# Kernel tuning notes

Measured on AMD Instinct MI355X. Metric: run time of the kernel, lower is better.

The kernel has to match this reference:

```python
import jax, jax.numpy as jnp
import numpy as np

N = 50000
IN_DIM = 512
HIDDEN = 64
OUT_DIM = 47
E1 = 800000
E2 = 1200000


def setup_inputs() -> dict:
    key = jax.random.key(0)
    ks = jax.random.split(key, 10)
    x = jax.random.normal(ks[0], (N, IN_DIM), dtype=jnp.float32)
    src1 = jax.random.randint(ks[1], (E1,), 0, N, dtype=jnp.int32)
    dst1 = jax.random.randint(ks[2], (E1,), 0, N, dtype=jnp.int32)
    w1 = jax.random.uniform(ks[3], (E1,), dtype=jnp.float32)
    src2 = jax.random.randint(ks[4], (E2,), 0, N, dtype=jnp.int32)
    dst2 = jax.random.randint(ks[5], (E2,), 0, N, dtype=jnp.int32)
    w2 = jax.random.uniform(ks[6], (E2,), dtype=jnp.float32)
    embed_w = jax.random.normal(ks[7], (IN_DIM, HIDDEN), dtype=jnp.float32) / np.sqrt(IN_DIM)
    embed_b = jnp.zeros((HIDDEN,), dtype=jnp.float32)
    total_dim = (2 ** 3 - 1) * HIDDEN  # k=2 -> 7*hidden
    cls_w = jax.random.normal(ks[8], (total_dim, OUT_DIM), dtype=jnp.float32) / np.sqrt(total_dim)
    cls_b = jnp.zeros((OUT_DIM,), dtype=jnp.float32)
    return {"x": x, "src1": src1, "dst1": dst1, "w1": w1,
            "src2": src2, "dst2": dst2, "w2": w2,
            "embed_w": embed_w, "embed_b": embed_b,
            "cls_w": cls_w, "cls_b": cls_b}


def _spmm(src, dst, w, h, n):
    # out[i] = sum_{e: dst[e]==i} w[e] * h[src[e]]  == sparse_adj @ h
    return jax.ops.segment_sum(w[:, None] * h[src], dst, num_segments=n)


def reference(x, src1, dst1, w1, src2, dst2, w2, embed_w, embed_b, cls_w, cls_b):
    k = 2
    # dropout is identity in eval mode
    h = jax.nn.relu(x @ embed_w + embed_b)  # [N, hidden]
    reps = [h]
    for _ in range(k):
        h1 = _spmm(src1, dst1, w1, h, N)  # strict 1-hop
        h2 = _spmm(src2, dst2, w2, h, N)  # strict 2-hop
        h = jax.nn.relu(jnp.concatenate([h1, h2], axis=1))
        reps.append(h)
    h_final = jnp.concatenate(reps, axis=1)  # [N, 7*hidden]
    return h_final @ cls_w + cls_b
```

## Files before the change

kernel.cpp:

```cpp
#include <hip/hip_runtime.h>

#define N_NODES 50000
#define IN_DIM 512
#define HIDDEN 64
#define OUT_DIM 47
#define HSTRIDE 448

#define NBINS 391
#define CAP1 3072
#define CAP2 4096
#define CHUNK 4096

typedef unsigned short u16;
typedef short v8s __attribute__((ext_vector_type(8)));
typedef float v4f __attribute__((ext_vector_type(4)));

union F4 { float4 v; float f[4]; };
union U4 { uint4 v; unsigned u[4]; };

static __device__ __forceinline__ u16 f2bf(float f) {
  unsigned u = __float_as_uint(f);
  u += 0x7fffu + ((u >> 16) & 1u);
  return (u16)(u >> 16);
}
static __device__ __forceinline__ float bf2f(u16 h) {
  return __uint_as_float(((unsigned)h) << 16);
}

__global__ __launch_bounds__(256) void prep_scatter(
    const float* __restrict__ embed_w, u16* __restrict__ weTh,
    u16* __restrict__ weTl, const float* __restrict__ cls_w,
    u16* __restrict__ wcTh, u16* __restrict__ wcTl,
    const int* __restrict__ src1, const int* __restrict__ dst1,
    const float* __restrict__ w1, int E1, int c1,
    const int* __restrict__ src2, const int* __restrict__ dst2,
    const float* __restrict__ w2, int E2,
    int* __restrict__ binCursor, int2* __restrict__ stg1,
    int2* __restrict__ stg2) {
  int b = blockIdx.x;
  if (b < 16) {
    int tid = b * 256 + threadIdx.x;
    int col = tid >> 6;
    int k8 = (tid & 63) * 8;
#pragma unroll
    for (int j = 0; j < 8; j++) {
      float v = embed_w[(size_t)(k8 + j) * HIDDEN + col];
      u16 h = f2bf(v);
      weTh[(size_t)col * IN_DIM + k8 + j] = h;
      weTl[(size_t)col * IN_DIM + k8 + j] = f2bf(v - bf2f(h));
    }
    return;
  }
  if (b < 27) {
    int tid = (b - 16) * 256 + threadIdx.x;
    if (tid < 48 * 56) {
      int col = tid / 56;
      int k8 = (tid % 56) * 8;
#pragma unroll
      for (int j = 0; j < 8; j++) {
        float v = (col < OUT_DIM) ? cls_w[(size_t)(k8 + j) * OUT_DIM + col] : 0.f;
        u16 h = f2bf(v);
        wcTh[(size_t)col * HSTRIDE + k8 + j] = h;
        wcTl[(size_t)col * HSTRIDE + k8 + j] = f2bf(v - bf2f(h));
      }
    }
    return;
  }

  int q = b - 27;
  const int *src, *dst;
  const float* w;
  int E, cap;
  int2* stg;
  int* bc;
  if (q < c1) {
    src = src1; dst = dst1; w = w1; E = E1; stg = stg1; bc = binCursor; cap = CAP1;
  } else {
    q -= c1;
    src = src2; dst = dst2; w = w2; E = E2; stg = stg2; bc = binCursor + NBINS; cap = CAP2;
  }
  int e0 = q * CHUNK;
  int n = E - e0;
  if (n > CHUNK) n = CHUNK;

  __shared__ int hist[NBINS], segrel[NBINS], cur[NBINS];
  for (int i = threadIdx.x; i < NBINS; i += 256) { hist[i] = 0; cur[i] = 0; }
  __syncthreads();
  for (int t = threadIdx.x; t < n; t += 256)
    atomicAdd(&hist[dst[e0 + t] >> 7], 1);
  __syncthreads();
  for (int i = threadIdx.x; i < NBINS; i += 256) {
    int h = hist[i];
    segrel[i] = h ? atomicAdd(&bc[i], h) : 0;
  }
  __syncthreads();
  for (int t = threadIdx.x; t < n; t += 256) {
    int d = dst[e0 + t];
    int bin = d >> 7;
    int rel = segrel[bin] + atomicAdd(&cur[bin], 1);
    if (rel < cap)
      stg[(size_t)bin * cap + rel] =
          make_int2(src[e0 + t] | ((d & 127) << 16), __float_as_int(w[e0 + t]));
  }
}

__global__ __launch_bounds__(512) void binscan(const int* __restrict__ cnt,
                                               int* __restrict__ scanout) {
  const int* in = cnt + blockIdx.x * NBINS;
  int* out = scanout + blockIdx.x * NBINS;
  int tid = threadIdx.x, lane = tid & 63, wid = tid >> 6;
  __shared__ int wsum[8];
  int v0 = (tid < NBINS) ? in[tid] : 0;
  int v = v0;
#pragma unroll
  for (int off = 1; off < 64; off <<= 1) {
    int t = __shfl_up(v, off, 64);
    if (lane >= off) v += t;
  }
  if (lane == 63) wsum[wid] = v;
  __syncthreads();
  if (tid < 8) {
    int s = wsum[tid], sc = s;
#pragma unroll
    for (int off = 1; off < 8; off <<= 1) {
      int t = __shfl_up(sc, off, 8);
      if (tid >= off) sc += t;
    }
    wsum[tid] = sc - s;
  }
  __syncthreads();
  if (tid < NBINS) out[tid] = v - v0 + wsum[wid];
}

__global__ __launch_bounds__(256) void embed_place(
    const float* __restrict__ x, const u16* __restrict__ wTh,
    const u16* __restrict__ wTl, const float* __restrict__ bias,
    u16* __restrict__ hcat, const int* __restrict__ binCursor,
    const int* __restrict__ binScan, const int2* __restrict__ stg1,
    int2* __restrict__ ew1, int* __restrict__ ep1,
    const int2* __restrict__ stg2, int2* __restrict__ ew2,
    int* __restrict__ ep2) {
  int b = blockIdx.x;
  if (b < 782) {
    int wave = threadIdx.x >> 6, lane = threadIdx.x & 63;
    int row0 = b * 64 + wave * 16;
    int m = lane & 15, kq = lane >> 4;
    int rowA = row0 + m;
    if (rowA >= N_NODES) rowA = N_NODES - 1;
    const float* xr = x + (size_t)rowA * IN_DIM;

    v4f acc[4];
#pragma unroll
    for (int nf = 0; nf < 4; nf++) acc[nf] = (v4f){0.f, 0.f, 0.f, 0.f};

#pragma unroll 4
    for (int k0 = 0; k0 < IN_DIM; k0 += 32) {
      int kk = k0 + kq * 8;
      F4 p, qv;
      p.v = *(const float4*)(xr + kk);
      qv.v = *(const float4*)(xr + kk + 4);
      v8s a;
#pragma unroll
      for (int j = 0; j < 4; j++) {
        a[j] = (short)f2bf(p.f[j]);
        a[4 + j] = (short)f2bf(qv.f[j]);
      }
#pragma unroll
      for (int nf = 0; nf < 4; nf++) {
        int col = nf * 16 + m;
        v8s bh = *(const v8s*)(wTh + (size_t)col * IN_DIM + kk);
        v8s bl = *(const v8s*)(wTl + (size_t)col * IN_DIM + kk);
        acc[nf] = __builtin_amdgcn_mfma_f32_16x16x32_bf16(a, bh, acc[nf], 0, 0, 0);
        acc[nf] = __builtin_amdgcn_mfma_f32_16x16x32_bf16(a, bl, acc[nf], 0, 0, 0);
      }
    }

#pragma unroll
    for (int nf = 0; nf < 4; nf++) {
      int col = nf * 16 + m;
      float bv = bias[col];
#pragma unroll
      for (int reg = 0; reg < 4; reg++) {
        int rowC = row0 + kq * 4 + reg;
        if (rowC < N_NODES) {
          float v = acc[nf][reg] + bv;
          hcat[(size_t)rowC * HSTRIDE + col] = f2bf(v > 0.f ? v : 0.f);
        }
      }
    }
    return;
  }

  int bin = b - 782;
  int lb = bin < NBINS ? bin : bin - NBINS;
  const int2* stg;
  int2* ew;
  int* ep;
  int cap;
  if (bin < NBINS) { stg = stg1; ew = ew1; ep = ep1; cap = CAP1; }
  else             { stg = stg2; ew = ew2; ep = ep2; cap = CAP2; }
  int cnt = binCursor[bin];
  if (cnt > cap) cnt = cap;
  int base = binScan[bin];
  const int2* seg = stg + (size_t)lb * cap;
  int node0 = lb << 7;
  int nnodes = N_NODES - node0;
  if (nnodes > 128) nnodes = 128;

  __shared__ int ncnt[128], noff[128], ncur[128];
  __shared__ int t0;
  if (threadIdx.x < 128) { ncnt[threadIdx.x] = 0; ncur[threadIdx.x] = 0; }
  __syncthreads();
  for (int t = threadIdx.x; t < cnt; t += 256)
    atomicAdd(&ncnt[(seg[t].x >> 16) & 127], 1);
  __syncthreads();
  int v0 = 0, v = 0;
  if (threadIdx.x < 128) {
    v0 = ncnt[threadIdx.x];
    v = v0;
    int lane = threadIdx.x & 63;
#pragma unroll
    for (int off = 1; off < 64; off <<= 1) {
      int t = __shfl_up(v, off, 64);
      if (lane >= off) v += t;
    }
    if (threadIdx.x == 63) t0 = v;
  }
  __syncthreads();
  if (threadIdx.x < 128) {
    int excl = v - v0 + (threadIdx.x >= 64 ? t0 : 0);
    noff[threadIdx.x] = excl;
    if (threadIdx.x < nnodes) ep[node0 + threadIdx.x] = base + excl + v0;
  }
  __syncthreads();
  for (int t = threadIdx.x; t < cnt; t += 256) {
    int2 pk = seg[t];
    int nl = (pk.x >> 16) & 127;
    int pos = base + noff[nl] + atomicAdd(&ncur[nl], 1);
    ew[pos] = make_int2(pk.x & 0xFFFF, pk.y);
  }
}

__device__ __forceinline__ void bf8_fma(const U4& r, float wt, float* a) {
#pragma unroll
  for (int i = 0; i < 4; i++) {
    a[2 * i]     += wt * __uint_as_float(r.u[i] << 16);
    a[2 * i + 1] += wt * __uint_as_float(r.u[i] & 0xffff0000u);
  }
}

template <int NT>
__global__ __launch_bounds__(256) void gather2(
    const int* __restrict__ ep1, const int2* __restrict__ ew1,
    const int* __restrict__ ep2, const int2* __restrict__ ew2,
    const u16* __restrict__ hin, u16* __restrict__ out1,
    u16* __restrict__ out2, int half_blocks) {
  int b = blockIdx.x;
  const int* ep;
  const int2* ew;
  u16* out;
  if (b < half_blocks) { ep = ep1; ew = ew1; out = out1; }
  else { b -= half_blocks; ep = ep2; ew = ew2; out = out2; }

  int tid = b * 256 + threadIdx.x;
  int node = tid / NT;
  if (node >= N_NODES) return;
  int col0 = (tid % NT) * 8;
  int s = node ? ep[node - 1] : 0;
  int e = ep[node];

  float a0[8], a1[8];
#pragma unroll
  for (int i = 0; i < 8; i++) { a0[i] = 0.f; a1[i] = 0.f; }

  int j = s;
  for (; j + 4 <= e; j += 4) {
    int2 p0 = ew[j], p1 = ew[j + 1], p2 = ew[j + 2], p3 = ew[j + 3];
    U4 r0, r1, r2, r3;
    r0.v = *(const uint4*)(hin + (size_t)p0.x * HSTRIDE + col0);
    r1.v = *(const uint4*)(hin + (size_t)p1.x * HSTRIDE + col0);
    r2.v = *(const uint4*)(hin + (size_t)p2.x * HSTRIDE + col0);
    r3.v = *(const uint4*)(hin + (size_t)p3.x * HSTRIDE + col0);
    bf8_fma(r0, __int_as_float(p0.y), a0);
    bf8_fma(r1, __int_as_float(p1.y), a1);
    bf8_fma(r2, __int_as_float(p2.y), a0);
    bf8_fma(r3, __int_as_float(p3.y), a1);
  }
  for (; j < e; j++) {
    int2 p = ew[j];
    U4 r;
    r.v = *(const uint4*)(hin + (size_t)p.x * HSTRIDE + col0);
    bf8_fma(r, __int_as_float(p.y), a0);
  }

  U4 o;
#pragma unroll
  for (int i = 0; i < 4; i++) {
    float lo = a0[2 * i] + a1[2 * i];
    float hi = a0[2 * i + 1] + a1[2 * i + 1];
    lo = lo > 0.f ? lo : 0.f;
    hi = hi > 0.f ? hi : 0.f;
    o.u[i] = ((unsigned)f2bf(hi) << 16) | (unsigned)f2bf(lo);
  }
  *(uint4*)(out + (size_t)node * HSTRIDE + col0) = o.v;
}

__global__ __launch_bounds__(256) void final_mfma(
    const u16* __restrict__ hcat, const u16* __restrict__ wTh,
    const u16* __restrict__ wTl, const float* __restrict__ bias,
    float* __restrict__ out) {
  int wave = threadIdx.x >> 6, lane = threadIdx.x & 63;
  int row0 = blockIdx.x * 64 + wave * 16;
  int m = lane & 15, kq = lane >> 4;
  int rowA = row0 + m;
  if (rowA >= N_NODES) rowA = N_NODES - 1;
  const u16* hr = hcat + (size_t)rowA * HSTRIDE;

  v4f acc[3];
#pragma unroll
  for (int nf = 0; nf < 3; nf++) acc[nf] = (v4f){0.f, 0.f, 0.f, 0.f};

#pragma unroll 2
  for (int k0 = 0; k0 < HSTRIDE; k0 += 32) {
    int kk = k0 + kq * 8;
    v8s a = *(const v8s*)(hr + kk);
#pragma unroll
    for (int nf = 0; nf < 3; nf++) {
      int col = nf * 16 + m;
      v8s bh = *(const v8s*)(wTh + (size_t)col * HSTRIDE + kk);
      v8s bl = *(const v8s*)(wTl + (size_t)col * HSTRIDE + kk);
      acc[nf] = __builtin_amdgcn_mfma_f32_16x16x32_bf16(a, bh, acc[nf], 0, 0, 0);
      acc[nf] = __builtin_amdgcn_mfma_f32_16x16x32_bf16(a, bl, acc[nf], 0, 0, 0);
    }
  }

#pragma unroll
  for (int nf = 0; nf < 3; nf++) {
    int col = nf * 16 + m;
    if (col < OUT_DIM) {
      float bv = bias[col];
#pragma unroll
      for (int reg = 0; reg < 4; reg++) {
        int rowC = row0 + kq * 4 + reg;
        if (rowC < N_NODES)
          out[(size_t)rowC * OUT_DIM + col] = acc[nf][reg] + bv;
      }
    }
  }
}

extern "C" void kernel_launch(void* const* d_in, const int* in_sizes, int n_in,
                              void* d_out, int out_size, void* d_ws,
                              size_t ws_size, hipStream_t stream) {
  const float* x       = (const float*)d_in[0];
  const int*   src1    = (const int*)d_in[1];
  const int*   dst1    = (const int*)d_in[2];
  const float* w1      = (const float*)d_in[3];
  const int*   src2    = (const int*)d_in[4];
  const int*   dst2    = (const int*)d_in[5];
  const float* w2      = (const float*)d_in[6];
  const float* embed_w = (const float*)d_in[7];
  const float* embed_b = (const float*)d_in[8];
  const float* cls_w   = (const float*)d_in[9];
  const float* cls_b   = (const float*)d_in[10];
  int E1 = in_sizes[1];
  int E2 = in_sizes[4];

  float* ws = (float*)d_ws;
  size_t off = 0;
  u16* hcat = (u16*)(ws + off); off += (size_t)N_NODES * HSTRIDE / 2;
  int2* ew1 = (int2*)(ws + off); off += (size_t)2 * E1;
  int2* ew2 = (int2*)(ws + off); off += (size_t)2 * E2;
  int* ep1 = (int*)(ws + off); off += N_NODES;
  int* ep2 = (int*)(ws + off); off += N_NODES;
  int2* stg1 = (int2*)(ws + off); off += (size_t)2 * NBINS * CAP1;
  int2* stg2 = (int2*)(ws + off); off += (size_t)2 * NBINS * CAP2;
  int* binCursor = (int*)(ws + off); off += 2 * NBINS;
  int* binScan = (int*)(ws + off); off += 2 * NBINS;
  u16* weTh = (u16*)(ws + off); off += 16384;
  u16* weTl = (u16*)(ws + off); off += 16384;
  u16* wcTh = (u16*)(ws + off); off += 10752;
  u16* wcTl = (u16*)(ws + off); off += 10752;

  int c1 = (E1 + CHUNK - 1) / CHUNK;
  int c2 = (E2 + CHUNK - 1) / CHUNK;

  hipMemsetAsync(binCursor, 0, 2 * NBINS * sizeof(int), stream);
  prep_scatter<<<27 + c1 + c2, 256, 0, stream>>>(
      embed_w, weTh, weTl, cls_w, wcTh, wcTl,
      src1, dst1, w1, E1, c1, src2, dst2, w2, E2,
      binCursor, stg1, stg2);
  binscan<<<2, 512, 0, stream>>>(binCursor, binScan);
  embed_place<<<782 + 2 * NBINS, 256, 0, stream>>>(
      x, weTh, weTl, embed_b, hcat, binCursor, binScan,
      stg1, ew1, ep1, stg2, ew2, ep2);
  gather2<8><<<3126, 256, 0, stream>>>(ep1, ew1, ep2, ew2, hcat,
                                       hcat + 64, hcat + 128, 1563);
  gather2<16><<<6250, 256, 0, stream>>>(ep1, ew1, ep2, ew2, hcat + 64,
                                        hcat + 192, hcat + 320, 3125);
  final_mfma<<<782, 256, 0, stream>>>(hcat, wcTh, wcTl, cls_b, (float*)d_out);
}
```

Baseline: 259.8 us.

## Regroup kernels so embedding GEMM overlaps edge binning instead of placement

Moves the weight conversion into its own small kernel. The embedding MFMA GEMM now shares a launch with the edge-scatter binning pass instead of the placement pass, and placement becomes a standalone kernel. The goal is to overlap the compute-heavy embedding with the larger atomic-heavy binning phase and shorten the placement stage. It adds one kernel launch and changes which work shares the GPU at each stage.

```diff
diff --git a/kernel.cpp b/kernel.cpp
--- a/kernel.cpp
+++ b/kernel.cpp
@@ -27,10 +27,42 @@
   return __uint_as_float(((unsigned)h) << 16);
 }
 
-__global__ __launch_bounds__(256) void prep_scatter(
+__global__ __launch_bounds__(256) void conv_w(
     const float* __restrict__ embed_w, u16* __restrict__ weTh,
     u16* __restrict__ weTl, const float* __restrict__ cls_w,
-    u16* __restrict__ wcTh, u16* __restrict__ wcTl,
+    u16* __restrict__ wcTh, u16* __restrict__ wcTl) {
+  int b = blockIdx.x;
+  if (b < 16) {
+    int tid = b * 256 + threadIdx.x;
+    int col = tid >> 6;
+    int k8 = (tid & 63) * 8;
+#pragma unroll
+    for (int j = 0; j < 8; j++) {
+      float v = embed_w[(size_t)(k8 + j) * HIDDEN + col];
+      u16 h = f2bf(v);
+      weTh[(size_t)col * IN_DIM + k8 + j] = h;
+      weTl[(size_t)col * IN_DIM + k8 + j] = f2bf(v - bf2f(h));
+    }
+  } else {
+    int tid = (b - 16) * 256 + threadIdx.x;
+    if (tid < 48 * 56) {
+      int col = tid / 56;
+      int k8 = (tid % 56) * 8;
+#pragma unroll
+      for (int j = 0; j < 8; j++) {
+        float v = (col < OUT_DIM) ? cls_w[(size_t)(k8 + j) * OUT_DIM + col] : 0.f;
+        u16 h = f2bf(v);
+        wcTh[(size_t)col * HSTRIDE + k8 + j] = h;
+        wcTl[(size_t)col * HSTRIDE + k8 + j] = f2bf(v - bf2f(h));
+      }
+    }
+  }
+}
+
+__global__ __launch_bounds__(256) void embed_bin(
+    const float* __restrict__ x, const u16* __restrict__ wTh,
+    const u16* __restrict__ wTl, const float* __restrict__ bias,
+    u16* __restrict__ hcat,
     const int* __restrict__ src1, const int* __restrict__ dst1,
     const float* __restrict__ w1, int E1, int c1,
     const int* __restrict__ src2, const int* __restrict__ dst2,
@@ -38,36 +70,57 @@
     int* __restrict__ binCursor, int2* __restrict__ stg1,
     int2* __restrict__ stg2) {
   int b = blockIdx.x;
-  if (b < 16) {
-    int tid = b * 256 + threadIdx.x;
-    int col = tid >> 6;
-    int k8 = (tid & 63) * 8;
-#pragma unroll
-    for (int j = 0; j < 8; j++) {
-      float v = embed_w[(size_t)(k8 + j) * HIDDEN + col];
-      u16 h = f2bf(v);
-      weTh[(size_t)col * IN_DIM + k8 + j] = h;
-      weTl[(size_t)col * IN_DIM + k8 + j] = f2bf(v - bf2f(h));
+  if (b < 782) {
+    int wave = threadIdx.x >> 6, lane = threadIdx.x & 63;
+    int row0 = b * 64 + wave * 16;
+    int m = lane & 15, kq = lane >> 4;
+    int rowA = row0 + m;
+    if (rowA >= N_NODES) rowA = N_NODES - 1;
+    const float* xr = x + (size_t)rowA * IN_DIM;
+
+    v4f acc[4];
+#pragma unroll
+    for (int nf = 0; nf < 4; nf++) acc[nf] = (v4f){0.f, 0.f, 0.f, 0.f};
+
+#pragma unroll 4
+    for (int k0 = 0; k0 < IN_DIM; k0 += 32) {
+      int kk = k0 + kq * 8;
+      F4 p, qv;
+      p.v = *(const float4*)(xr + kk);
+      qv.v = *(const float4*)(xr + kk + 4);
+      v8s a;
+#pragma unroll
+      for (int j = 0; j < 4; j++) {
+        a[j] = (short)f2bf(p.f[j]);
+        a[4 + j] = (short)f2bf(qv.f[j]);
+      }
+#pragma unroll
+      for (int nf = 0; nf < 4; nf++) {
+        int col = nf * 16 + m;
+        v8s bh = *(const v8s*)(wTh + (size_t)col * IN_DIM + kk);
+        v8s bl = *(const v8s*)(wTl + (size_t)col * IN_DIM + kk);
+        acc[nf] = __builtin_amdgcn_mfma_f32_16x16x32_bf16(a, bh, acc[nf], 0, 0, 0);
+        acc[nf] = __builtin_amdgcn_mfma_f32_16x16x32_bf16(a, bl, acc[nf], 0, 0, 0);
+      }
+    }
+
+#pragma unroll
+    for (int nf = 0; nf < 4; nf++) {
+      int col = nf * 16 + m;
+      float bv = bias[col];
+#pragma unroll
+      for (int reg = 0; reg < 4; reg++) {
+        int rowC = row0 + kq * 4 + reg;
+        if (rowC < N_NODES) {
+          float v = acc[nf][reg] + bv;
+          hcat[(size_t)rowC * HSTRIDE + col] = f2bf(v > 0.f ? v : 0.f);
+        }
+      }
     }
     return;
   }
-  if (b < 27) {
-    int tid = (b - 16) * 256 + threadIdx.x;
-    if (tid < 48 * 56) {
-      int col = tid / 56;
-      int k8 = (tid % 56) * 8;
-#pragma unroll
-      for (int j = 0; j < 8; j++) {
-        float v = (col < OUT_DIM) ? cls_w[(size_t)(k8 + j) * OUT_DIM + col] : 0.f;
-        u16 h = f2bf(v);
-        wcTh[(size_t)col * HSTRIDE + k8 + j] = h;
-        wcTl[(size_t)col * HSTRIDE + k8 + j] = f2bf(v - bf2f(h));
-      }
-    }
-    return;
-  }
-
-  int q = b - 27;
+
+  int q = b - 782;
   const int *src, *dst;
   const float* w;
   int E, cap;
@@ -132,76 +185,22 @@
   if (tid < NBINS) out[tid] = v - v0 + wsum[wid];
 }
 
-__global__ __launch_bounds__(256) void embed_place(
-    const float* __restrict__ x, const u16* __restrict__ wTh,
-    const u16* __restrict__ wTl, const float* __restrict__ bias,
-    u16* __restrict__ hcat, const int* __restrict__ binCursor,
-    const int* __restrict__ binScan, const int2* __restrict__ stg1,
-    int2* __restrict__ ew1, int* __restrict__ ep1,
-    const int2* __restrict__ stg2, int2* __restrict__ ew2,
-    int* __restrict__ ep2) {
-  int b = blockIdx.x;
-  if (b < 782) {
-    int wave = threadIdx.x >> 6, lane = threadIdx.x & 63;
-    int row0 = b * 64 + wave * 16;
-    int m = lane & 15, kq = lane >> 4;
-    int rowA = row0 + m;
-    if (rowA >= N_NODES) rowA = N_NODES - 1;
-    const float* xr = x + (size_t)rowA * IN_DIM;
-
-    v4f acc[4];
-#pragma unroll
-    for (int nf = 0; nf < 4; nf++) acc[nf] = (v4f){0.f, 0.f, 0.f, 0.f};
-
-#pragma unroll 4
-    for (int k0 = 0; k0 < IN_DIM; k0 += 32) {
-      int kk = k0 + kq * 8;
-      F4 p, qv;
-      p.v = *(const float4*)(xr + kk);
-      qv.v = *(const float4*)(xr + kk + 4);
-      v8s a;
-#pragma unroll
-      for (int j = 0; j < 4; j++) {
-        a[j] = (short)f2bf(p.f[j]);
-        a[4 + j] = (short)f2bf(qv.f[j]);
-      }
-#pragma unroll
-      for (int nf = 0; nf < 4; nf++) {
-        int col = nf * 16 + m;
-        v8s bh = *(const v8s*)(wTh + (size_t)col * IN_DIM + kk);
-        v8s bl = *(const v8s*)(wTl + (size_t)col * IN_DIM + kk);
-        acc[nf] = __builtin_amdgcn_mfma_f32_16x16x32_bf16(a, bh, acc[nf], 0, 0, 0);
-        acc[nf] = __builtin_amdgcn_mfma_f32_16x16x32_bf16(a, bl, acc[nf], 0, 0, 0);
-      }
-    }
-
-#pragma unroll
-    for (int nf = 0; nf < 4; nf++) {
-      int col = nf * 16 + m;
-      float bv = bias[col];
-#pragma unroll
-      for (int reg = 0; reg < 4; reg++) {
-        int rowC = row0 + kq * 4 + reg;
-        if (rowC < N_NODES) {
-          float v = acc[nf][reg] + bv;
-          hcat[(size_t)rowC * HSTRIDE + col] = f2bf(v > 0.f ? v : 0.f);
-        }
-      }
-    }
-    return;
-  }
-
-  int bin = b - 782;
-  int lb = bin < NBINS ? bin : bin - NBINS;
+__global__ __launch_bounds__(256) void place(
+    const int* __restrict__ binCursor, const int* __restrict__ binScan,
+    const int2* __restrict__ stg1, int2* __restrict__ ew1,
+    int* __restrict__ ep1, const int2* __restrict__ stg2,
+    int2* __restrict__ ew2, int* __restrict__ ep2) {
+  int pb = blockIdx.x;
+  int lb = pb < NBINS ? pb : pb - NBINS;
   const int2* stg;
   int2* ew;
   int* ep;
   int cap;
-  if (bin < NBINS) { stg = stg1; ew = ew1; ep = ep1; cap = CAP1; }
-  else             { stg = stg2; ew = ew2; ep = ep2; cap = CAP2; }
-  int cnt = binCursor[bin];
+  if (pb < NBINS) { stg = stg1; ew = ew1; ep = ep1; cap = CAP1; }
+  else            { stg = stg2; ew = ew2; ep = ep2; cap = CAP2; }
+  int cnt = binCursor[pb];
   if (cnt > cap) cnt = cap;
-  int base = binScan[bin];
+  int base = binScan[pb];
   const int2* seg = stg + (size_t)lb * cap;
   int node0 = lb << 7;
   int nnodes = N_NODES - node0;
@@ -386,14 +385,14 @@
   int c2 = (E2 + CHUNK - 1) / CHUNK;
 
   hipMemsetAsync(binCursor, 0, 2 * NBINS * sizeof(int), stream);
-  prep_scatter<<<27 + c1 + c2, 256, 0, stream>>>(
-      embed_w, weTh, weTl, cls_w, wcTh, wcTl,
+  conv_w<<<27, 256, 0, stream>>>(embed_w, weTh, weTl, cls_w, wcTh, wcTl);
+  embed_bin<<<782 + c1 + c2, 256, 0, stream>>>(
+      x, weTh, weTl, embed_b, hcat,
       src1, dst1, w1, E1, c1, src2, dst2, w2, E2,
       binCursor, stg1, stg2);
   binscan<<<2, 512, 0, stream>>>(binCursor, binScan);
-  embed_place<<<782 + 2 * NBINS, 256, 0, stream>>>(
-      x, weTh, weTl, embed_b, hcat, binCursor, binScan,
-      stg1, ew1, ep1, stg2, ew2, ep2);
+  place<<<2 * NBINS, 256, 0, stream>>>(binCursor, binScan,
+                                       stg1, ew1, ep1, stg2, ew2, ep2);
   gather2<8><<<3126, 256, 0, stream>>>(ep1, ew1, ep2, ew2, hcat,
                                        hcat + 64, hcat + 128, 1563);
   gather2<16><<<6250, 256, 0, stream>>>(ep1, ew1, ep2, ew2, hcat + 64,
```

After: 260.7 us. Within noise of the previous version (+0.3%).
